# Kernel optimization log

Hardware: AMD Instinct MI355X
Metric: run time of the kernel (lower is better)

## Reference

```python
import math
import jax, jax.numpy as jnp
import numpy as np

CANVAS_SHAPE = (256, 256)
NUM_SAMPLES = 32
MAX_LENGTH = 300.0
EPSILON = 1e-6


def _bezier_eval(cp, ts):
    # cp: [K, 2] control points, ts: [S] -> [S, 2] via Bernstein basis
    K = cp.shape[0]
    n = K - 1
    i = jnp.arange(K)
    binom = jnp.asarray([math.comb(n, k) for k in range(K)], dtype=cp.dtype)
    t = ts[:, None].astype(cp.dtype)  # [S, 1]
    basis = binom * (t ** i) * ((1.0 - t) ** (n - i))  # [S, K]
    return basis @ cp


def _decasteljau_left(cp, t):
    # Control points of the sub-curve on [0, t] (left de Casteljau subdivision).
    K = cp.shape[0]
    pts = cp
    left = [cp[0]]
    for _ in range(K - 1):
        pts = (1.0 - t) * pts[:-1] + t * pts[1:]
        left.append(pts[0])
    return jnp.stack(left)


def setup_inputs() -> dict:
    key = jax.random.key(0)
    k1, k2, k3 = jax.random.split(key, 3)
    B, K = 16, 4
    inputs = jax.random.uniform(k1, (B, K, 2), dtype=jnp.float32)  # normalized keypoints
    widths = jax.random.uniform(k2, (B,), dtype=jnp.float32) * 6.0 + 2.0  # stroke widths in px
    aa_factors = jax.random.uniform(k3, (B,), dtype=jnp.float32) * 2.0 + 1.0  # anti-alias exponents
    return {"inputs": inputs, "widths": widths, "aa_factors": aa_factors}


def reference(inputs, widths, aa_factors):
    H, W = CANVAS_SHAPE
    canvas_dims = jnp.asarray([H, W], dtype=inputs.dtype)
    key_points = inputs * canvas_dims[None, None, :]  # [B, K, 2]
    ts = jnp.linspace(0.0, 1.0, NUM_SAMPLES)

    def per_curve_samples(cp):
        # arc length approximated with NUM_SAMPLES piecewise-linear segments
        approx = _bezier_eval(cp, ts)  # [S, 2]
        seg = approx[1:] - approx[:-1]
        arc_len = jnp.sum(jnp.sqrt(jnp.sum(seg * seg, axis=-1)))
        # truncate curve to max_length if too long (no-op when arc_len <= MAX_LENGTH)
        t_trunc = jnp.minimum(1.0, MAX_LENGTH / (arc_len + EPSILON))
        cp_trunc = _decasteljau_left(cp, t_trunc)
        return _bezier_eval(cp_trunc, ts)  # [S, 2]

    sample_points = jax.vmap(per_curve_samples)(key_points)  # [B, S, 2]

    yy, xx = jnp.meshgrid(jnp.arange(H), jnp.arange(W), indexing="ij")
    positions = jnp.stack([yy, xx], axis=-1).reshape(-1, 2).astype(inputs.dtype)  # [HW, 2] as (y, x)

    # pairwise pixel-to-sample distances, min over samples (memory-bound reduction)
    diff = positions[None, None, :, :] - sample_points[:, :, None, :]  # [B, S, HW, 2]
    dists = jnp.sqrt(jnp.sum(diff * diff, axis=-1))  # [B, S, HW]
    min_d = jnp.min(dists, axis=1)  # [B, HW]

    canvas = 1.0 - (min_d / widths[:, None] + EPSILON) ** aa_factors[:, None]
    return jnp.clip(canvas, 0.0, 1.0).reshape(-1, H, W)
```

## Files before the change

### kernel.cpp

```cpp
#include <hip/hip_runtime.h>


constexpr int CH = 256, CW = 256;
constexpr int S = 32;
constexpr int NB = 16;
constexpr int BLK = 256;
constexpr int TILE = 32;
constexpr float MAXLEN = 300.0f;
constexpr float EPS = 1e-6f;

__device__ inline float2 bez4(const float2 cp[4], float t) {
    float u = 1.0f - t;
    float b0 = u * u * u;
    float b1 = 3.0f * u * u * t;
    float b2 = 3.0f * u * t * t;
    float b3 = t * t * t;
    float2 r;
    r.x = b0 * cp[0].x + b1 * cp[1].x + b2 * cp[2].x + b3 * cp[3].x;
    r.y = b0 * cp[0].y + b1 * cp[1].y + b2 * cp[2].y + b3 * cp[3].y;
    return r;
}

__device__ inline float shade(float m, float wd, float aa) {
    float md = sqrtf(m);
    float base = md / wd + EPS;
    float v = 1.0f - __expf(aa * __logf(base));
    return fminf(fmaxf(v, 0.0f), 1.0f);
}

__global__ __launch_bounds__(BLK) void curve_kernel(
    const float* __restrict__ inp,
    const float* __restrict__ widths,
    const float* __restrict__ aas,
    float* __restrict__ out)
{
    const int b = blockIdx.z;
    const int tx0 = blockIdx.x * TILE;
    const int ty0 = blockIdx.y * TILE;
    const int tid = threadIdx.x;

    __shared__ float2 s_samp[S];
    __shared__ float2 s_cp[4];
    __shared__ int s_active;

    float2 cp[4];
    if (tid < S) {
#pragma unroll
        for (int k = 0; k < 4; ++k) {
            cp[k].x = inp[(b * 4 + k) * 2 + 0] * 256.0f;
            cp[k].y = inp[(b * 4 + k) * 2 + 1] * 256.0f;
        }
        float t = (float)tid * (1.0f / 31.0f);
        s_samp[tid] = bez4(cp, t);
    }
    __syncthreads();

    if (tid == 0) {
        float arc = 0.0f;
        for (int j = 0; j < S - 1; ++j) {
            float dy = s_samp[j + 1].x - s_samp[j].x;
            float dx = s_samp[j + 1].y - s_samp[j].y;
            arc += sqrtf(dy * dy + dx * dx);
        }
        float tt = fminf(1.0f, MAXLEN / (arc + EPS));
        float u = 1.0f - tt;
        float2 a01, a12, a23, q0, q1, c0;
        a01.x = u * cp[0].x + tt * cp[1].x;  a01.y = u * cp[0].y + tt * cp[1].y;
        a12.x = u * cp[1].x + tt * cp[2].x;  a12.y = u * cp[1].y + tt * cp[2].y;
        a23.x = u * cp[2].x + tt * cp[3].x;  a23.y = u * cp[2].y + tt * cp[3].y;
        q0.x = u * a01.x + tt * a12.x;       q0.y = u * a01.y + tt * a12.y;
        q1.x = u * a12.x + tt * a23.x;       q1.y = u * a12.y + tt * a23.y;
        c0.x = u * q0.x + tt * q1.x;         c0.y = u * q0.y + tt * q1.y;
        s_cp[0] = cp[0]; s_cp[1] = a01; s_cp[2] = q0; s_cp[3] = c0;
    }
    __syncthreads();

    if (tid < S) {
        float2 cpl[4] = { s_cp[0], s_cp[1], s_cp[2], s_cp[3] };
        float t = (float)tid * (1.0f / 31.0f);
        s_samp[tid] = bez4(cpl, t);
    }
    __syncthreads();

    const float wd = widths[b];
    bool pred = false;
    if (tid < S) {
        float2 sp = s_samp[tid];
        float dyl = fmaxf(0.0f, fmaxf((float)ty0 - sp.x, sp.x - (float)(ty0 + TILE - 1)));
        float dxl = fmaxf(0.0f, fmaxf((float)tx0 - sp.y, sp.y - (float)(tx0 + TILE - 1)));
        pred = fmaf(dxl, dxl, dyl * dyl) < wd * wd;
    }
    unsigned long long mask = __ballot(pred);
    if (tid == 0) s_active = (mask != 0ULL);
    __syncthreads();

    const int row = ty0 + (tid >> 3);
    const int col = tx0 + (tid & 7) * 4;
    float* dst = out + b * (CH * CW) + row * CW + col;

    if (!s_active) {
        float4 z = make_float4(0.0f, 0.0f, 0.0f, 0.0f);
        *reinterpret_cast<float4*>(dst) = z;
        return;
    }

    const float aa = aas[b];
    const float fy = (float)row;
    const float fx = (float)col;

    float m0 = 1e30f, m1 = 1e30f, m2 = 1e30f, m3 = 1e30f;
#pragma unroll
    for (int j = 0; j < S; ++j) {
        float2 sp = s_samp[j];
        float dy = fy - sp.x;
        float dy2 = dy * dy;
        float dx0 = fx - sp.y;
        float dx1 = fx + 1.0f - sp.y;
        float dx2 = fx + 2.0f - sp.y;
        float dx3 = fx + 3.0f - sp.y;
        m0 = fminf(m0, fmaf(dx0, dx0, dy2));
        m1 = fminf(m1, fmaf(dx1, dx1, dy2));
        m2 = fminf(m2, fmaf(dx2, dx2, dy2));
        m3 = fminf(m3, fmaf(dx3, dx3, dy2));
    }

    float4 o;
    o.x = shade(m0, wd, aa);
    o.y = shade(m1, wd, aa);
    o.z = shade(m2, wd, aa);
    o.w = shade(m3, wd, aa);
    *reinterpret_cast<float4*>(dst) = o;
}

extern "C" void kernel_launch(void* const* d_in, const int* in_sizes, int n_in,
                              void* d_out, int out_size, void* d_ws, size_t ws_size,
                              hipStream_t stream) {
    const float* inp = (const float*)d_in[0];
    const float* widths = (const float*)d_in[1];
    const float* aas = (const float*)d_in[2];
    float* out = (float*)d_out;

    dim3 grid(CW / TILE, CH / TILE, NB);
    curve_kernel<<<grid, BLK, 0, stream>>>(inp, widths, aas, out);
}
```

Baseline: 64.03 us.

## Compute curve samples per wavefront with shuffles, drop shared memory and barriers

Every wavefront now evaluates the 32 Bezier samples in registers, one per lane with lanes 32-63 duplicating them. It computes the arc length with a shuffle reduction, halved because of that duplication, and does the de Casteljau truncation redundantly in each lane. This removes three __syncthreads barriers, the serial single-thread arc-length loop and the shared-memory sample array. The distance loop broadcasts samples with readlane, so values come through scalar registers. The cost is redundant per-lane setup math, and correctness relies on the 64-wide wavefront assumption.

```diff
diff --git a/kernel.cpp b/kernel.cpp
--- a/kernel.cpp
+++ b/kernel.cpp
@@ -9,16 +9,15 @@
 constexpr float MAXLEN = 300.0f;
 constexpr float EPS = 1e-6f;
 
-__device__ inline float2 bez4(const float2 cp[4], float t) {
+__device__ inline void bez4v(const float cy[4], const float cx[4], float t,
+                             float& ry, float& rx) {
     float u = 1.0f - t;
     float b0 = u * u * u;
     float b1 = 3.0f * u * u * t;
     float b2 = 3.0f * u * t * t;
     float b3 = t * t * t;
-    float2 r;
-    r.x = b0 * cp[0].x + b1 * cp[1].x + b2 * cp[2].x + b3 * cp[3].x;
-    r.y = b0 * cp[0].y + b1 * cp[1].y + b2 * cp[2].y + b3 * cp[3].y;
-    return r;
+    ry = b0 * cy[0] + b1 * cy[1] + b2 * cy[2] + b3 * cy[3];
+    rx = b0 * cx[0] + b1 * cx[1] + b2 * cx[2] + b3 * cx[3];
 }
 
 __device__ inline float shade(float m, float wd, float aa) {
@@ -38,69 +37,53 @@
     const int tx0 = blockIdx.x * TILE;
     const int ty0 = blockIdx.y * TILE;
     const int tid = threadIdx.x;
+    const int sj = tid & 31;
 
-    __shared__ float2 s_samp[S];
-    __shared__ float2 s_cp[4];
-    __shared__ int s_active;
+    float cy[4], cx[4];
+#pragma unroll
+    for (int k = 0; k < 4; ++k) {
+        cy[k] = inp[(b * 4 + k) * 2 + 0] * 256.0f;
+        cx[k] = inp[(b * 4 + k) * 2 + 1] * 256.0f;
+    }
+    const float wd = widths[b];
 
-    float2 cp[4];
-    if (tid < S) {
+    const float t = (float)sj * (1.0f / 31.0f);
+    float py, px;
+    bez4v(cy, cx, t, py, px);
+
+    float nyy = __shfl_down(py, 1);
+    float nxx = __shfl_down(px, 1);
+    float dsy = nyy - py, dsx = nxx - px;
+    float seg = (sj < 31) ? sqrtf(dsy * dsy + dsx * dsx) : 0.0f;
 #pragma unroll
-        for (int k = 0; k < 4; ++k) {
-            cp[k].x = inp[(b * 4 + k) * 2 + 0] * 256.0f;
-            cp[k].y = inp[(b * 4 + k) * 2 + 1] * 256.0f;
-        }
-        float t = (float)tid * (1.0f / 31.0f);
-        s_samp[tid] = bez4(cp, t);
-    }
-    __syncthreads();
+    for (int m = 1; m < 64; m <<= 1) seg += __shfl_xor(seg, m);
+    const float arc = 0.5f * seg;
 
-    if (tid == 0) {
-        float arc = 0.0f;
-        for (int j = 0; j < S - 1; ++j) {
-            float dy = s_samp[j + 1].x - s_samp[j].x;
-            float dx = s_samp[j + 1].y - s_samp[j].y;
-            arc += sqrtf(dy * dy + dx * dx);
-        }
-        float tt = fminf(1.0f, MAXLEN / (arc + EPS));
-        float u = 1.0f - tt;
-        float2 a01, a12, a23, q0, q1, c0;
-        a01.x = u * cp[0].x + tt * cp[1].x;  a01.y = u * cp[0].y + tt * cp[1].y;
-        a12.x = u * cp[1].x + tt * cp[2].x;  a12.y = u * cp[1].y + tt * cp[2].y;
-        a23.x = u * cp[2].x + tt * cp[3].x;  a23.y = u * cp[2].y + tt * cp[3].y;
-        q0.x = u * a01.x + tt * a12.x;       q0.y = u * a01.y + tt * a12.y;
-        q1.x = u * a12.x + tt * a23.x;       q1.y = u * a12.y + tt * a23.y;
-        c0.x = u * q0.x + tt * q1.x;         c0.y = u * q0.y + tt * q1.y;
-        s_cp[0] = cp[0]; s_cp[1] = a01; s_cp[2] = q0; s_cp[3] = c0;
-    }
-    __syncthreads();
+    const float tt = fminf(1.0f, MAXLEN / (arc + EPS));
+    const float u = 1.0f - tt;
+    float a01y = u * cy[0] + tt * cy[1], a01x = u * cx[0] + tt * cx[1];
+    float a12y = u * cy[1] + tt * cy[2], a12x = u * cx[1] + tt * cx[2];
+    float a23y = u * cy[2] + tt * cy[3], a23x = u * cx[2] + tt * cx[3];
+    float q0y = u * a01y + tt * a12y,   q0x = u * a01x + tt * a12x;
+    float q1y = u * a12y + tt * a23y,   q1x = u * a12x + tt * a23x;
+    float c0y = u * q0y + tt * q1y,     c0x = u * q0x + tt * q1x;
+    float ly[4] = { cy[0], a01y, q0y, c0y };
+    float lx[4] = { cx[0], a01x, q0x, c0x };
 
-    if (tid < S) {
-        float2 cpl[4] = { s_cp[0], s_cp[1], s_cp[2], s_cp[3] };
-        float t = (float)tid * (1.0f / 31.0f);
-        s_samp[tid] = bez4(cpl, t);
-    }
-    __syncthreads();
+    float spy, spx;
+    bez4v(ly, lx, t, spy, spx);
 
-    const float wd = widths[b];
-    bool pred = false;
-    if (tid < S) {
-        float2 sp = s_samp[tid];
-        float dyl = fmaxf(0.0f, fmaxf((float)ty0 - sp.x, sp.x - (float)(ty0 + TILE - 1)));
-        float dxl = fmaxf(0.0f, fmaxf((float)tx0 - sp.y, sp.y - (float)(tx0 + TILE - 1)));
-        pred = fmaf(dxl, dxl, dyl * dyl) < wd * wd;
-    }
+    float dyl = fmaxf(0.0f, fmaxf((float)ty0 - spy, spy - (float)(ty0 + TILE - 1)));
+    float dxl = fmaxf(0.0f, fmaxf((float)tx0 - spx, spx - (float)(tx0 + TILE - 1)));
+    bool pred = fmaf(dxl, dxl, dyl * dyl) < wd * wd;
     unsigned long long mask = __ballot(pred);
-    if (tid == 0) s_active = (mask != 0ULL);
-    __syncthreads();
 
     const int row = ty0 + (tid >> 3);
     const int col = tx0 + (tid & 7) * 4;
     float* dst = out + b * (CH * CW) + row * CW + col;
 
-    if (!s_active) {
-        float4 z = make_float4(0.0f, 0.0f, 0.0f, 0.0f);
-        *reinterpret_cast<float4*>(dst) = z;
+    if (mask == 0ULL) {
+        *reinterpret_cast<float4*>(dst) = make_float4(0.0f, 0.0f, 0.0f, 0.0f);
         return;
     }
 
@@ -111,13 +94,16 @@
     float m0 = 1e30f, m1 = 1e30f, m2 = 1e30f, m3 = 1e30f;
 #pragma unroll
     for (int j = 0; j < S; ++j) {
-        float2 sp = s_samp[j];
-        float dy = fy - sp.x;
+        float sy = __uint_as_float(
+            (unsigned)__builtin_amdgcn_readlane((int)__float_as_uint(spy), j));
+        float sx = __uint_as_float(
+            (unsigned)__builtin_amdgcn_readlane((int)__float_as_uint(spx), j));
+        float dy  = fy - sy;
         float dy2 = dy * dy;
-        float dx0 = fx - sp.y;
-        float dx1 = fx + 1.0f - sp.y;
-        float dx2 = fx + 2.0f - sp.y;
-        float dx3 = fx + 3.0f - sp.y;
+        float dx0 = fx - sx;
+        float dx1 = fx + 1.0f - sx;
+        float dx2 = fx + 2.0f - sx;
+        float dx3 = fx + 3.0f - sx;
         m0 = fminf(m0, fmaf(dx0, dx0, dy2));
         m1 = fminf(m1, fmaf(dx1, dx1, dy2));
         m2 = fminf(m2, fmaf(dx2, dx2, dy2));
```

New measurement: 63.02 us. About the same (-1.6%).
